# Performance work log

Measured on AMD Instinct MI355X. Metric: run time of the kernel, lower is better.

The kernel has to match this reference:

```python
import jax, jax.numpy as jnp
import numpy as np

NODE_DIM = 256
OUT_DIM = 512
NUM_HEADS = 8
HEAD_DIM = 32
HID = NUM_HEADS * HEAD_DIM  # 256
N_NODES = 200000
N_GRAPHS = 2000


def _linear_init(key, fan_in, fan_out):
    lim = 1.0 / np.sqrt(fan_in)
    kw, kb = jax.random.split(key)
    w = jax.random.uniform(kw, (fan_in, fan_out), minval=-lim, maxval=lim, dtype=jnp.float32)
    b = jax.random.uniform(kb, (fan_out,), minval=-lim, maxval=lim, dtype=jnp.float32)
    return w, b


def setup_inputs() -> dict:
    key = jax.random.key(0)
    ks = jax.random.split(key, 16)
    inp = {}
    inp["node_embeddings"] = jax.random.normal(ks[0], (N_NODES, NODE_DIM), dtype=jnp.float32)
    inp["node_to_graph_id"] = jnp.sort(jax.random.randint(ks[1], (N_NODES,), 0, N_GRAPHS)).astype(jnp.int64)
    inp["num_graphs"] = N_GRAPHS
    # weighted_mean pooler params
    inp["wm_score_w1"], inp["wm_score_b1"] = _linear_init(ks[2], NODE_DIM, HID)
    inp["wm_score_w2"], inp["wm_score_b2"] = _linear_init(ks[3], HID, NUM_HEADS)
    inp["wm_val_w1"], inp["wm_val_b1"] = _linear_init(ks[4], NODE_DIM, HID)
    inp["wm_val_w2"], inp["wm_val_b2"] = _linear_init(ks[5], HID, NUM_HEADS * HEAD_DIM)
    inp["wm_comb_w"] = _linear_init(ks[6], NUM_HEADS * HEAD_DIM, OUT_DIM)[0]
    # weighted_sum pooler params
    inp["ws_score_w1"], inp["ws_score_b1"] = _linear_init(ks[7], NODE_DIM, HID)
    inp["ws_score_w2"], inp["ws_score_b2"] = _linear_init(ks[8], HID, NUM_HEADS)
    inp["ws_val_w1"], inp["ws_val_b1"] = _linear_init(ks[9], NODE_DIM, HID)
    inp["ws_val_w2"], inp["ws_val_b2"] = _linear_init(ks[10], HID, NUM_HEADS * HEAD_DIM)
    inp["ws_comb_w"] = _linear_init(ks[11], NUM_HEADS * HEAD_DIM, OUT_DIM)[0]
    # max pooler + final combination
    inp["mx_comb_w"] = _linear_init(ks[12], NODE_DIM, OUT_DIM)[0]
    inp["final_w"] = _linear_init(ks[13], 3 * OUT_DIM, OUT_DIM)[0]
    return inp


def _mlp(x, w1, b1, w2, b2):
    return jax.nn.relu(x @ w1 + b1) @ w2 + b2


def _scatter_softmax(scores, seg, num_graphs):
    # scores: [N, H]; softmax over nodes within each graph, per head
    m = jax.ops.segment_max(scores, seg, num_segments=num_graphs)
    m = jnp.where(jnp.isfinite(m), m, 0.0)  # empty graphs
    e = jnp.exp(scores - m[seg])
    s = jax.ops.segment_sum(e, seg, num_segments=num_graphs)
    return e / s[seg]


def _multihead_readout(x, seg, num_graphs, sw1, sb1, sw2, sb2, vw1, vb1, vw2, vb2, cw, weighted_mean):
    scores = _mlp(x, sw1, sb1, sw2, sb2)                       # [N, heads]
    if weighted_mean:
        weights = _scatter_softmax(scores, seg, num_graphs)
    else:
        weights = jax.nn.sigmoid(scores)
    values = _mlp(x, vw1, vb1, vw2, vb2).reshape(-1, NUM_HEADS, HEAD_DIM)
    weighted = (weights[:, :, None] * values).reshape(-1, NUM_HEADS * HEAD_DIM)
    per_graph = jax.ops.segment_sum(weighted, seg, num_segments=num_graphs)
    return per_graph @ cw


def reference(node_embeddings, node_to_graph_id, num_graphs,
              wm_score_w1, wm_score_b1, wm_score_w2, wm_score_b2,
              wm_val_w1, wm_val_b1, wm_val_w2, wm_val_b2, wm_comb_w,
              ws_score_w1, ws_score_b1, ws_score_w2, ws_score_b2,
              ws_val_w1, ws_val_b1, ws_val_w2, ws_val_b2, ws_comb_w,
              mx_comb_w, final_w):
    seg = node_to_graph_id.astype(jnp.int32)
    mean_repr = _multihead_readout(node_embeddings, seg, num_graphs,
                                   wm_score_w1, wm_score_b1, wm_score_w2, wm_score_b2,
                                   wm_val_w1, wm_val_b1, wm_val_w2, wm_val_b2, wm_comb_w, True)
    sum_repr = _multihead_readout(node_embeddings, seg, num_graphs,
                                  ws_score_w1, ws_score_b1, ws_score_w2, ws_score_b2,
                                  ws_val_w1, ws_val_b1, ws_val_w2, ws_val_b2, ws_comb_w, False)
    pg_max = jax.ops.segment_max(node_embeddings, seg, num_segments=num_graphs)
    pg_max = jnp.where(jnp.isfinite(pg_max), pg_max, 0.0)  # torch_scatter zeros empty segments
    max_repr = pg_max @ mx_comb_w
    raw = jnp.concatenate([mean_repr, sum_repr, max_repr], axis=1)  # [G, 3*out_dim]
    return jax.nn.relu(raw) @ final_w
```

## Files before the change

kernel.cpp:

```cpp
#include <hip/hip_runtime.h>
#include <hip/hip_bf16.h>

typedef __bf16 bf16_t;
typedef __bf16 bf16x8 __attribute__((ext_vector_type(8)));
typedef float  f32x4  __attribute__((ext_vector_type(4)));

#define MFMA16(a, b, c) __builtin_amdgcn_mfma_f32_16x16x32_bf16((a), (b), (c), 0, 0, 0)

#define ROWS 48

__device__ __forceinline__ int gray(int row) { return (row ^ (row >> 1)) & 7; }
__device__ __forceinline__ int swz256(int row, int col) {
    return row * 256 + ((((col >> 3) ^ gray(row)) << 3) | (col & 7));
}

__device__ __forceinline__ bf16x8 cvt8(float4 a, float4 b) {
    bf16x8 o;
    o[0] = (bf16_t)a.x; o[1] = (bf16_t)a.y; o[2] = (bf16_t)a.z; o[3] = (bf16_t)a.w;
    o[4] = (bf16_t)b.x; o[5] = (bf16_t)b.y; o[6] = (bf16_t)b.z; o[7] = (bf16_t)b.w;
    return o;
}

__device__ __forceinline__ unsigned enc_max(float x) {
    unsigned b = __float_as_uint(x);
    return (b & 0x80000000u) ? ~b : (b | 0x80000000u);
}
__device__ __forceinline__ float dec_max(unsigned e) {
    if (e == 0u) return 0.0f;
    return (e & 0x80000000u) ? __uint_as_float(e ^ 0x80000000u) : __uint_as_float(~e);
}

__device__ __forceinline__ void gemm256p(const bf16_t* __restrict__ As,
                                         const bf16_t* __restrict__ Wk,
                                         f32x4 acc[3][2], int w, int l) {
    const int l15 = l & 15, hi = l >> 4;
#pragma unroll
    for (int mt = 0; mt < 3; ++mt)
#pragma unroll
        for (int j = 0; j < 2; ++j) acc[mt][j] = (f32x4){0.f, 0.f, 0.f, 0.f};

    const bf16_t* wb = Wk + ((size_t)hi * 256 + w * 32 + l15) * 8;

    bf16x8 b0[3], b1[3];
    bf16x8 a[2][3];
    b0[0] = *(const bf16x8*)(wb);
    b1[0] = *(const bf16x8*)(wb + 128);
    b0[1] = *(const bf16x8*)(wb + 8192);
    b1[1] = *(const bf16x8*)(wb + 8192 + 128);
#pragma unroll
    for (int mt = 0; mt < 3; ++mt) {
        const int row = mt * 16 + l15;
        a[0][mt] = *(const bf16x8*)(As + row * 256 + (hi ^ gray(row)) * 8);
    }

#pragma unroll
    for (int kt = 0; kt < 8; ++kt) {
        const int cur = kt % 3, nx2 = (kt + 2) % 3;
        if (kt + 2 < 8) {
            b0[nx2] = *(const bf16x8*)(wb + (kt + 2) * 8192);
            b1[nx2] = *(const bf16x8*)(wb + (kt + 2) * 8192 + 128);
        }
        if (kt + 1 < 8) {
#pragma unroll
            for (int mt = 0; mt < 3; ++mt) {
                const int row = mt * 16 + l15;
                a[(kt + 1) & 1][mt] =
                    *(const bf16x8*)(As + row * 256 + (((kt + 1) * 4 + hi) ^ gray(row)) * 8);
            }
        }
#pragma unroll
        for (int mt = 0; mt < 3; ++mt) {
            acc[mt][0] = MFMA16(a[kt & 1][mt], b0[cur], acc[mt][0]);
            acc[mt][1] = MFMA16(a[kt & 1][mt], b1[cur], acc[mt][1]);
        }
    }
}

__device__ __forceinline__ void write_h(f32x4 acc[3][2], const float* __restrict__ bias,
                                        bool relu, bf16_t* __restrict__ dst, int w, int l) {
    const int l15 = l & 15, hi = l >> 4;
#pragma unroll
    for (int j = 0; j < 2; ++j) {
        const int col = w * 32 + j * 16 + l15;
        const float bv = bias[col];
#pragma unroll
        for (int mt = 0; mt < 3; ++mt)
#pragma unroll
            for (int r = 0; r < 4; ++r) {
                const int row = mt * 16 + hi * 4 + r;
                float v = acc[mt][j][r] + bv;
                if (relu) v = fmaxf(v, 0.f);
                dst[swz256(row, col)] = (bf16_t)v;
            }
    }
}

__device__ __forceinline__ void gemm_score(const bf16_t* __restrict__ As,
                                           const bf16_t* __restrict__ W2k,
                                           const float* __restrict__ b2,
                                           float* __restrict__ ssc, int coloff, int w, int l) {
    if (w >= 3) return;
    const int l15 = l & 15, hi = l >> 4;
    const int row = w * 16 + l15;
    const bf16_t* wb = W2k + ((size_t)hi * 16 + l15) * 8;
    bf16x8 b[3];
    b[0] = *(const bf16x8*)(wb);
    b[1] = *(const bf16x8*)(wb + 512);
    f32x4 acc = (f32x4){0.f, 0.f, 0.f, 0.f};
#pragma unroll
    for (int kt = 0; kt < 8; ++kt) {
        const int cur = kt % 3, nx2 = (kt + 2) % 3;
        if (kt + 2 < 8) b[nx2] = *(const bf16x8*)(wb + (kt + 2) * 512);
        bf16x8 a = *(const bf16x8*)(As + row * 256 + ((kt * 4 + hi) ^ gray(row)) * 8);
        acc = MFMA16(a, b[cur], acc);
    }
    if (l15 < 8) {
        const float bv = b2[l15];
#pragma unroll
        for (int r = 0; r < 4; ++r) {
            const int orow = w * 16 + hi * 4 + r;
            ssc[orow * 16 + coloff + l15] = acc[r] + bv;
        }
    }
}

template <bool WM>
__device__ __forceinline__ void reduce_seg(const bf16_t* __restrict__ sh,
                                           const float* __restrict__ ssc,
                                           const bf16_t* __restrict__ sx,
                                           const int* __restrict__ sseg,
                                           float* __restrict__ num, float* __restrict__ den,
                                           unsigned* __restrict__ pmax, int G) {
    const int col = threadIdx.x & 255;
    const int rbeg = (threadIdx.x >> 8) * 24;
    float av = 0.f, ad = 0.f;
    unsigned am = 0u;
    int gcur = sseg[rbeg];
    for (int r = rbeg; r < rbeg + 24; ++r) {
        const int g = sseg[r];
        if (g != gcur) {
            if ((unsigned)gcur < (unsigned)G) {
                atomicAdd(&num[(size_t)gcur * 256 + col], av);
                if (WM) {
                    if (col < 8) atomicAdd(&den[(size_t)gcur * 8 + col], ad);
                    atomicMax(&pmax[(size_t)gcur * 256 + col], am);
                }
            }
            av = 0.f; ad = 0.f; am = 0u; gcur = g;
        }
        const int si = swz256(r, col);
        const float v = (float)sh[si];
        const float wgt = ssc[r * 16 + (WM ? 0 : 8) + (col >> 5)];
        av += wgt * v;
        if (WM) {
            if (col < 8) ad += ssc[r * 16 + col];
            am = max(am, enc_max((float)sx[si]));
        }
    }
    if ((unsigned)gcur < (unsigned)G) {
        atomicAdd(&num[(size_t)gcur * 256 + col], av);
        if (WM) {
            if (col < 8) atomicAdd(&den[(size_t)gcur * 8 + col], ad);
            atomicMax(&pmax[(size_t)gcur * 256 + col], am);
        }
    }
}

__global__ __launch_bounds__(512, 3) void node_kernel(
    const float* __restrict__ X, const int* __restrict__ seg,
    const bf16_t* __restrict__ wt_sw1_wm, const bf16_t* __restrict__ wt_sw2_wm,
    const bf16_t* __restrict__ wt_vw1_wm, const bf16_t* __restrict__ wt_vw2_wm,
    const bf16_t* __restrict__ wt_sw1_ws, const bf16_t* __restrict__ wt_sw2_ws,
    const bf16_t* __restrict__ wt_vw1_ws, const bf16_t* __restrict__ wt_vw2_ws,
    const float* __restrict__ b_sw1_wm, const float* __restrict__ b_sw2_wm,
    const float* __restrict__ b_vw1_wm, const float* __restrict__ b_vw2_wm,
    const float* __restrict__ b_sw1_ws, const float* __restrict__ b_sw2_ws,
    const float* __restrict__ b_vw1_ws, const float* __restrict__ b_vw2_ws,
    float* __restrict__ num_wm, float* __restrict__ den_wm,
    float* __restrict__ acc_ws, unsigned* __restrict__ pmax, int N, int G) {
    __shared__ __align__(16) bf16_t sx[ROWS * 256];
    __shared__ __align__(16) bf16_t sh[ROWS * 256];
    __shared__ float ssc[ROWS * 16];
    __shared__ int sseg[ROWS];

    const int tid = threadIdx.x;
    const int w = tid >> 6, l = tid & 63;
    const int r0 = blockIdx.x * ROWS;

#pragma unroll
    for (int i = 0; i < 3; ++i) {
        const int cid = tid + i * 512;
        const int row = cid >> 5, ch = cid & 31;
        bf16x8 o;
        if (r0 + row < N) {
            const float4* gp = (const float4*)(X + (size_t)(r0 + row) * 256 + ch * 8);
            o = cvt8(gp[0], gp[1]);
        } else {
            for (int j = 0; j < 8; ++j) o[j] = (bf16_t)0.f;
        }
        *(bf16x8*)(sx + row * 256 + (ch ^ gray(row)) * 8) = o;
    }
    if (tid < ROWS) sseg[tid] = (r0 + tid < N) ? seg[r0 + tid] : -1;
    __syncthreads();

    f32x4 acc[3][2];

    gemm256p(sx, wt_sw1_wm, acc, w, l);
    write_h(acc, b_sw1_wm, true, sh, w, l);
    __syncthreads();
    gemm_score(sh, wt_sw2_wm, b_sw2_wm, ssc, 0, w, l);
    __syncthreads();

    gemm256p(sx, wt_sw1_ws, acc, w, l);
    write_h(acc, b_sw1_ws, true, sh, w, l);
    __syncthreads();
    gemm_score(sh, wt_sw2_ws, b_sw2_ws, ssc, 8, w, l);
    __syncthreads();

#pragma unroll
    for (int i = 0; i < 2; ++i) {
        const int idx = tid + i * 512;
        if (idx < ROWS * 16) {
            const float v = ssc[idx];
            ssc[idx] = ((idx & 15) < 8) ? __expf(v) : 1.f / (1.f + __expf(-v));
        }
    }
    __syncthreads();

    gemm256p(sx, wt_vw1_wm, acc, w, l);
    write_h(acc, b_vw1_wm, true, sh, w, l);
    __syncthreads();
    gemm256p(sh, wt_vw2_wm, acc, w, l);
    __syncthreads();
    write_h(acc, b_vw2_wm, false, sh, w, l);
    __syncthreads();
    reduce_seg<true>(sh, ssc, sx, sseg, num_wm, den_wm, pmax, G);
    __syncthreads();

    gemm256p(sx, wt_vw1_ws, acc, w, l);
    write_h(acc, b_vw1_ws, true, sh, w, l);
    __syncthreads();
    gemm256p(sh, wt_vw2_ws, acc, w, l);
    __syncthreads();
    write_h(acc, b_vw2_ws, false, sx, w, l);
    __syncthreads();
    reduce_seg<false>(sx, ssc, sx, sseg, acc_ws, nullptr, nullptr, G);
}

__global__ __launch_bounds__(256, 2) void graph_kernel(
    const float* __restrict__ num_wm, const float* __restrict__ den_wm,
    const float* __restrict__ acc_ws, const unsigned* __restrict__ pmax,
    const bf16_t* __restrict__ wt_comb_wm, const bf16_t* __restrict__ wt_comb_ws,
    const bf16_t* __restrict__ wt_comb_mx, const bf16_t* __restrict__ wt_final,
    float* __restrict__ out, int G) {
    __shared__ __align__(16) bf16_t sa[16 * 256];
    __shared__ __align__(16) bf16_t sraw[16 * 1536];

    const int tid = threadIdx.x, w = tid >> 6, l = tid & 63;
    const int l15 = l & 15, hi = l >> 4;
    const int g0 = blockIdx.x * 16;

    for (int src = 0; src < 3; ++src) {
#pragma unroll
        for (int i = 0; i < 2; ++i) {
            const int cid = tid + i * 256;
            const int row = cid >> 5, ch = cid & 31;
            const int g = g0 + row;
            bf16x8 o;
            if (g < G) {
                if (src == 0) {
                    const float4* np = (const float4*)(num_wm + (size_t)g * 256 + ch * 8);
                    float4 v0 = np[0], v1 = np[1];
                    const float d = den_wm[(size_t)g * 8 + (ch >> 2)];
                    const float rd = (d > 0.f) ? 1.f / d : 0.f;
                    o[0] = (bf16_t)(v0.x * rd); o[1] = (bf16_t)(v0.y * rd);
                    o[2] = (bf16_t)(v0.z * rd); o[3] = (bf16_t)(v0.w * rd);
                    o[4] = (bf16_t)(v1.x * rd); o[5] = (bf16_t)(v1.y * rd);
                    o[6] = (bf16_t)(v1.z * rd); o[7] = (bf16_t)(v1.w * rd);
                } else if (src == 1) {
                    const float4* np = (const float4*)(acc_ws + (size_t)g * 256 + ch * 8);
                    o = cvt8(np[0], np[1]);
                } else {
                    const unsigned* mp = pmax + (size_t)g * 256 + ch * 8;
#pragma unroll
                    for (int j = 0; j < 8; ++j) o[j] = (bf16_t)dec_max(mp[j]);
                }
            } else {
                for (int j = 0; j < 8; ++j) o[j] = (bf16_t)0.f;
            }
            *(bf16x8*)(sa + row * 256 + (ch ^ gray(row)) * 8) = o;
        }
        __syncthreads();

        const bf16_t* Wt = (src == 0) ? wt_comb_wm : ((src == 1) ? wt_comb_ws : wt_comb_mx);
        bf16x8 a[8];
#pragma unroll
        for (int kt = 0; kt < 8; ++kt)
            a[kt] = *(const bf16x8*)(sa + l15 * 256 + ((kt * 4 + hi) ^ gray(l15)) * 8);
        f32x4 acc[8];
#pragma unroll
        for (int j = 0; j < 8; ++j) acc[j] = (f32x4){0.f, 0.f, 0.f, 0.f};
#pragma unroll
        for (int kt = 0; kt < 8; ++kt) {
            bf16x8 b[8];
#pragma unroll
            for (int j = 0; j < 8; ++j) {
                const int ncol = (w * 8 + j) * 16 + l15;
                b[j] = *(const bf16x8*)(Wt + ((size_t)(kt * 4 + hi) * 512 + ncol) * 8);
            }
#pragma unroll
            for (int j = 0; j < 8; ++j) acc[j] = MFMA16(a[kt], b[j], acc[j]);
        }
#pragma unroll
        for (int j = 0; j < 8; ++j) {
            const int col = src * 512 + (w * 8 + j) * 16 + l15;
#pragma unroll
            for (int r = 0; r < 4; ++r) {
                const int row = hi * 4 + r;
                const float v = fmaxf(acc[j][r], 0.f);
                sraw[row * 1536 + ((((col >> 3) ^ gray(row)) << 3) | (col & 7))] = (bf16_t)v;
            }
        }
        __syncthreads();
    }

    f32x4 facc[8];
#pragma unroll
    for (int j = 0; j < 8; ++j) facc[j] = (f32x4){0.f, 0.f, 0.f, 0.f};
    for (int kt = 0; kt < 48; ++kt) {
        bf16x8 a = *(const bf16x8*)(sraw + l15 * 1536 + ((kt * 4 + hi) ^ gray(l15)) * 8);
#pragma unroll
        for (int j = 0; j < 8; ++j) {
            const int ncol = (w * 8 + j) * 16 + l15;
            bf16x8 b = *(const bf16x8*)(wt_final + ((size_t)(kt * 4 + hi) * 512 + ncol) * 8);
            facc[j] = MFMA16(a, b, facc[j]);
        }
    }
#pragma unroll
    for (int j = 0; j < 8; ++j) {
        const int col = (w * 8 + j) * 16 + l15;
#pragma unroll
        for (int r = 0; r < 4; ++r) {
            const int row = hi * 4 + r;
            if (g0 + row < G) out[(size_t)(g0 + row) * 512 + col] = facc[j][r];
        }
    }
}

__global__ void prep_w(const float* __restrict__ src, bf16_t* __restrict__ dst,
                       int K, int N, int Nout) {
    const int idx = blockIdx.x * blockDim.x + threadIdx.x;
    const int total = K * Nout;
    if (idx >= total) return;
    const int j = idx & 7;
    const int rest = idx >> 3;
    const int n = rest % Nout;
    const int kc = rest / Nout;
    const int k = kc * 8 + j;
    const float v = (n < N) ? src[(size_t)k * N + n] : 0.f;
    dst[idx] = (bf16_t)v;
}

extern "C" void kernel_launch(void* const* d_in, const int* in_sizes, int n_in,
                              void* d_out, int out_size, void* d_ws, size_t ws_size,
                              hipStream_t stream) {
    const float* X = (const float*)d_in[0];
    const int* seg = (const int*)d_in[1];
    const int N = in_sizes[1];
    const int G = out_size / 512;

    float* num_wm = (float*)d_ws;
    float* acc_ws = num_wm + (size_t)G * 256;
    float* den_wm = acc_ws + (size_t)G * 256;
    unsigned* pmax = (unsigned*)(den_wm + (size_t)G * 8);
    bf16_t* wt = (bf16_t*)(pmax + (size_t)G * 256);

    bf16_t* wt_sw1_wm = wt;
    bf16_t* wt_sw2_wm = wt_sw1_wm + 65536;
    bf16_t* wt_vw1_wm = wt_sw2_wm + 4096;
    bf16_t* wt_vw2_wm = wt_vw1_wm + 65536;
    bf16_t* wt_sw1_ws = wt_vw2_wm + 65536;
    bf16_t* wt_sw2_ws = wt_sw1_ws + 65536;
    bf16_t* wt_vw1_ws = wt_sw2_ws + 4096;
    bf16_t* wt_vw2_ws = wt_vw1_ws + 65536;
    bf16_t* wt_comb_wm = wt_vw2_ws + 65536;
    bf16_t* wt_comb_ws = wt_comb_wm + 131072;
    bf16_t* wt_comb_mx = wt_comb_ws + 131072;
    bf16_t* wt_final = wt_comb_mx + 131072;

    const size_t accum_bytes = ((size_t)G * 256 * 3 + (size_t)G * 8) * 4;
    hipMemsetAsync(d_ws, 0, accum_bytes, stream);

    struct TT { int srcIdx; bf16_t* dst; int K, Nn, Nout; };
    const TT tt[12] = {
        {3,  wt_sw1_wm, 256, 256, 256},  {5,  wt_sw2_wm, 256, 8,   16},
        {7,  wt_vw1_wm, 256, 256, 256},  {9,  wt_vw2_wm, 256, 256, 256},
        {12, wt_sw1_ws, 256, 256, 256},  {14, wt_sw2_ws, 256, 8,   16},
        {16, wt_vw1_ws, 256, 256, 256},  {18, wt_vw2_ws, 256, 256, 256},
        {11, wt_comb_wm, 256, 512, 512}, {20, wt_comb_ws, 256, 512, 512},
        {21, wt_comb_mx, 256, 512, 512}, {22, wt_final, 1536, 512, 512},
    };
    for (int i = 0; i < 12; ++i) {
        const int total = tt[i].Nout * tt[i].K;
        prep_w<<<(total + 255) / 256, 256, 0, stream>>>(
            (const float*)d_in[tt[i].srcIdx], tt[i].dst, tt[i].K, tt[i].Nn, tt[i].Nout);
    }

    const int nb = (N + ROWS - 1) / ROWS;
    node_kernel<<<nb, 512, 0, stream>>>(
        X, seg,
        wt_sw1_wm, wt_sw2_wm, wt_vw1_wm, wt_vw2_wm,
        wt_sw1_ws, wt_sw2_ws, wt_vw1_ws, wt_vw2_ws,
        (const float*)d_in[4], (const float*)d_in[6], (const float*)d_in[8], (const float*)d_in[10],
        (const float*)d_in[13], (const float*)d_in[15], (const float*)d_in[17], (const float*)d_in[19],
        num_wm, den_wm, acc_ws, pmax, N, G);

    const int gb = (G + 15) / 16;
    graph_kernel<<<gb, 256, 0, stream>>>(num_wm, den_wm, acc_ws, pmax,
                                         wt_comb_wm, wt_comb_ws, wt_comb_mx, wt_final,
                                         (float*)d_out, G);
}
```

Before: 320.5 us.

## Shrink node tile to 32 rows and merge weight prep launches into one

Lowers rows per node block from 48 to 32, which cuts shared memory and accumulator registers per block so more blocks can be resident and the grid grows. The GEMM, score, reduce and load loops are resized to match. Separately, the twelve per-matrix weight conversion launches become one kernel that looks up its matrix from a table, removing launch overhead. Smaller tiles reload the weight fragments more often per node and issue more segment atomics at block boundaries.

```diff
diff --git a/kernel.cpp b/kernel.cpp
--- a/kernel.cpp
+++ b/kernel.cpp
@@ -7,7 +7,7 @@
 
 #define MFMA16(a, b, c) __builtin_amdgcn_mfma_f32_16x16x32_bf16((a), (b), (c), 0, 0, 0)
 
-#define ROWS 48
+#define ROWS 32
 
 __device__ __forceinline__ int gray(int row) { return (row ^ (row >> 1)) & 7; }
 __device__ __forceinline__ int swz256(int row, int col) {
@@ -32,23 +32,23 @@
 
 __device__ __forceinline__ void gemm256p(const bf16_t* __restrict__ As,
                                          const bf16_t* __restrict__ Wk,
-                                         f32x4 acc[3][2], int w, int l) {
+                                         f32x4 acc[2][2], int w, int l) {
     const int l15 = l & 15, hi = l >> 4;
 #pragma unroll
-    for (int mt = 0; mt < 3; ++mt)
+    for (int mt = 0; mt < 2; ++mt)
 #pragma unroll
         for (int j = 0; j < 2; ++j) acc[mt][j] = (f32x4){0.f, 0.f, 0.f, 0.f};
 
     const bf16_t* wb = Wk + ((size_t)hi * 256 + w * 32 + l15) * 8;
 
     bf16x8 b0[3], b1[3];
-    bf16x8 a[2][3];
+    bf16x8 a[2][2];
     b0[0] = *(const bf16x8*)(wb);
     b1[0] = *(const bf16x8*)(wb + 128);
     b0[1] = *(const bf16x8*)(wb + 8192);
     b1[1] = *(const bf16x8*)(wb + 8192 + 128);
 #pragma unroll
-    for (int mt = 0; mt < 3; ++mt) {
+    for (int mt = 0; mt < 2; ++mt) {
         const int row = mt * 16 + l15;
         a[0][mt] = *(const bf16x8*)(As + row * 256 + (hi ^ gray(row)) * 8);
     }
@@ -62,21 +62,21 @@
         }
         if (kt + 1 < 8) {
 #pragma unroll
-            for (int mt = 0; mt < 3; ++mt) {
+            for (int mt = 0; mt < 2; ++mt) {
                 const int row = mt * 16 + l15;
                 a[(kt + 1) & 1][mt] =
                     *(const bf16x8*)(As + row * 256 + (((kt + 1) * 4 + hi) ^ gray(row)) * 8);
             }
         }
 #pragma unroll
-        for (int mt = 0; mt < 3; ++mt) {
+        for (int mt = 0; mt < 2; ++mt) {
             acc[mt][0] = MFMA16(a[kt & 1][mt], b0[cur], acc[mt][0]);
             acc[mt][1] = MFMA16(a[kt & 1][mt], b1[cur], acc[mt][1]);
         }
     }
 }
 
-__device__ __forceinline__ void write_h(f32x4 acc[3][2], const float* __restrict__ bias,
+__device__ __forceinline__ void write_h(f32x4 acc[2][2], const float* __restrict__ bias,
                                         bool relu, bf16_t* __restrict__ dst, int w, int l) {
     const int l15 = l & 15, hi = l >> 4;
 #pragma unroll
@@ -84,7 +84,7 @@
         const int col = w * 32 + j * 16 + l15;
         const float bv = bias[col];
 #pragma unroll
-        for (int mt = 0; mt < 3; ++mt)
+        for (int mt = 0; mt < 2; ++mt)
 #pragma unroll
             for (int r = 0; r < 4; ++r) {
                 const int row = mt * 16 + hi * 4 + r;
@@ -99,7 +99,7 @@
                                            const bf16_t* __restrict__ W2k,
                                            const float* __restrict__ b2,
                                            float* __restrict__ ssc, int coloff, int w, int l) {
-    if (w >= 3) return;
+    if (w >= 2) return;
     const int l15 = l & 15, hi = l >> 4;
     const int row = w * 16 + l15;
     const bf16_t* wb = W2k + ((size_t)hi * 16 + l15) * 8;
@@ -132,11 +132,11 @@
                                            float* __restrict__ num, float* __restrict__ den,
                                            unsigned* __restrict__ pmax, int G) {
     const int col = threadIdx.x & 255;
-    const int rbeg = (threadIdx.x >> 8) * 24;
+    const int rbeg = (threadIdx.x >> 8) * 16;
     float av = 0.f, ad = 0.f;
     unsigned am = 0u;
     int gcur = sseg[rbeg];
-    for (int r = rbeg; r < rbeg + 24; ++r) {
+    for (int r = rbeg; r < rbeg + 16; ++r) {
         const int g = sseg[r];
         if (g != gcur) {
             if ((unsigned)gcur < (unsigned)G) {
@@ -188,7 +188,7 @@
     const int r0 = blockIdx.x * ROWS;
 
 #pragma unroll
-    for (int i = 0; i < 3; ++i) {
+    for (int i = 0; i < 2; ++i) {
         const int cid = tid + i * 512;
         const int row = cid >> 5, ch = cid & 31;
         bf16x8 o;
@@ -203,7 +203,7 @@
     if (tid < ROWS) sseg[tid] = (r0 + tid < N) ? seg[r0 + tid] : -1;
     __syncthreads();
 
-    f32x4 acc[3][2];
+    f32x4 acc[2][2];
 
     gemm256p(sx, wt_sw1_wm, acc, w, l);
     write_h(acc, b_sw1_wm, true, sh, w, l);
@@ -217,13 +217,9 @@
     gemm_score(sh, wt_sw2_ws, b_sw2_ws, ssc, 8, w, l);
     __syncthreads();
 
-#pragma unroll
-    for (int i = 0; i < 2; ++i) {
-        const int idx = tid + i * 512;
-        if (idx < ROWS * 16) {
-            const float v = ssc[idx];
-            ssc[idx] = ((idx & 15) < 8) ? __expf(v) : 1.f / (1.f + __expf(-v));
-        }
+    {
+        const float v = ssc[tid];
+        ssc[tid] = ((tid & 15) < 8) ? __expf(v) : 1.f / (1.f + __expf(-v));
     }
     __syncthreads();
 
@@ -347,18 +343,28 @@
     }
 }
 
-__global__ void prep_w(const float* __restrict__ src, bf16_t* __restrict__ dst,
-                       int K, int N, int Nout) {
+struct PrepTab {
+    const float* src[12];
+    bf16_t* dst[12];
+    int K[12], Nn[12], Nout[12];
+    int base[13];
+};
+
+__global__ void prep_all(PrepTab t) {
     const int idx = blockIdx.x * blockDim.x + threadIdx.x;
-    const int total = K * Nout;
-    if (idx >= total) return;
-    const int j = idx & 7;
-    const int rest = idx >> 3;
-    const int n = rest % Nout;
-    const int kc = rest / Nout;
+    if (idx >= t.base[12]) return;
+    int i = 0;
+#pragma unroll
+    for (int s = 0; s < 12; ++s)
+        if (idx >= t.base[s + 1]) i = s + 1;
+    const int local = idx - t.base[i];
+    const int j = local & 7;
+    const int rest = local >> 3;
+    const int n = rest % t.Nout[i];
+    const int kc = rest / t.Nout[i];
     const int k = kc * 8 + j;
-    const float v = (n < N) ? src[(size_t)k * N + n] : 0.f;
-    dst[idx] = (bf16_t)v;
+    const float v = (n < t.Nn[i]) ? t.src[i][(size_t)k * t.Nn[i] + n] : 0.f;
+    t.dst[i][local] = (bf16_t)v;
 }
 
 extern "C" void kernel_launch(void* const* d_in, const int* in_sizes, int n_in,
@@ -400,11 +406,17 @@
         {11, wt_comb_wm, 256, 512, 512}, {20, wt_comb_ws, 256, 512, 512},
         {21, wt_comb_mx, 256, 512, 512}, {22, wt_final, 1536, 512, 512},
     };
+    PrepTab pt;
+    int base = 0;
     for (int i = 0; i < 12; ++i) {
-        const int total = tt[i].Nout * tt[i].K;
-        prep_w<<<(total + 255) / 256, 256, 0, stream>>>(
-            (const float*)d_in[tt[i].srcIdx], tt[i].dst, tt[i].K, tt[i].Nn, tt[i].Nout);
-    }
+        pt.src[i] = (const float*)d_in[tt[i].srcIdx];
+        pt.dst[i] = tt[i].dst;
+        pt.K[i] = tt[i].K; pt.Nn[i] = tt[i].Nn; pt.Nout[i] = tt[i].Nout;
+        pt.base[i] = base;
+        base += tt[i].K * tt[i].Nout;
+    }
+    pt.base[12] = base;
+    prep_all<<<(base + 255) / 256, 256, 0, stream>>>(pt);
 
     const int nb = (N + ROWS - 1) / ROWS;
     node_kernel<<<nb, 512, 0, stream>>>(
```

Measured after the change: 325.6 us. Within noise of the previous version (+1.6%).
